# Kernel tuning notes

Hardware: AMD Instinct MI355X
Metric: run time of the kernel (lower is better)

Reference implementation:

```python
import jax, jax.numpy as jnp
import numpy as np


def setup_inputs() -> dict:
    key = jax.random.key(0)
    k1, k2 = jax.random.split(key)
    B, C, H, W = 8, 64, 128, 256
    left_feature = jax.random.normal(k1, (B, C, H, W), dtype=jnp.float32)
    right_feature = jax.random.normal(k2, (B, C, H, W), dtype=jnp.float32)
    return {
        "left_feature": left_feature,
        "right_feature": right_feature,
        "max_disp": 64,
    }


def reference(left_feature, right_feature, max_disp):
    # Stereo correlation cost volume (norm=False branch):
    #   volume[b, d, h, w] = mean_c( left[b,c,h,w] * right[b,c,h,w-d] )  for w >= d
    #   volume[b, d, h, w] = 0                                           for w <  d
    b, c, h, w = left_feature.shape

    def corr_at_disp(d):
        # left[:, :, :, d:] * right[:, :, :, :w-d], mean over channel dim
        prod = left_feature[:, :, :, d:] * right_feature[:, :, :, : w - d]
        cv = jnp.mean(prod, axis=1)  # (b, h, w-d)
        # left-pad along width with zeros for invalid disparities
        return jnp.pad(cv, ((0, 0), (0, 0), (d, 0)))

    # max_disp is a static Python int; loop over disparity hyperparameter is static.
    volume = jnp.stack([corr_at_disp(d) for d in range(max_disp)], axis=1)
    return volume  # (b, max_disp, h, w)
```

## Files before the change

kernel.cpp:

```cpp
#include <hip/hip_runtime.h>

typedef _Float16 half8 __attribute__((ext_vector_type(8)));
typedef float floatx4 __attribute__((ext_vector_type(4)));

#define BB 8
#define CC 64
#define HH 128
#define WW 256
#define DD 64
#define KCH 32
#define LROWS WW
#define RROWS (WW + 64)

__global__ __launch_bounds__(256, 3)
void corr_volume_mfma(const float* __restrict__ left,
                      const float* __restrict__ right,
                      float* __restrict__ out) {
    __shared__ _Float16 Lb[LROWS * KCH];
    __shared__ _Float16 Rb[RROWS * KCH];

    const int tid  = threadIdx.x;
    const int lane = tid & 63;
    const int wv   = tid >> 6;
    const int n    = lane & 15;
    const int q    = lane >> 4;
    const int bh   = blockIdx.x;
    const int b    = bh >> 7;
    const int h    = bh & 127;

    const size_t chanStride = (size_t)HH * WW;
    const size_t rowBase    = (size_t)b * CC * chanStride + (size_t)h * WW;

    {
        half8 z;
        #pragma unroll
        for (int t = 0; t < 8; ++t) z[t] = (_Float16)0.0f;
        *(half8*)&Rb[tid * 8] = z;
    }

    floatx4 acc[4][5];
    #pragma unroll
    for (int t = 0; t < 4; ++t)
        #pragma unroll
        for (int u = 0; u < 5; ++u)
            #pragma unroll
            for (int r = 0; r < 4; ++r)
                acc[t][u][r] = 0.0f;

    const int wbase = wv * 64;
    const float* lcol = left  + rowBase + tid;
    const float* rcol = right + rowBase + tid;

    for (int ck = 0; ck < 2; ++ck) {
        __syncthreads();
        const int cb = ck * KCH;
        _Float16* Lrow = &Lb[tid * KCH];
        _Float16* Rrow = &Rb[(tid + 64) * KCH];
        #pragma unroll
        for (int g = 0; g < 4; ++g) {
            float lv[8], rv[8];
            #pragma unroll
            for (int t = 0; t < 8; ++t) {
                lv[t] = lcol[(size_t)(cb + g * 8 + t) * chanStride];
                rv[t] = rcol[(size_t)(cb + g * 8 + t) * chanStride];
            }
            half8 lh, rh;
            #pragma unroll
            for (int t = 0; t < 8; ++t) {
                lh[t] = (_Float16)lv[t];
                rh[t] = (_Float16)rv[t];
            }
            *(half8*)&Lrow[g * 8] = lh;
            *(half8*)&Rrow[g * 8] = rh;
        }
        __syncthreads();

        half8 bfrag[4], afrag[8];
        #pragma unroll
        for (int t = 0; t < 4; ++t)
            bfrag[t] = *(const half8*)&Lb[(wbase + t * 16 + n) * KCH + q * 8];
        #pragma unroll
        for (int a = 0; a < 8; ++a)
            afrag[a] = *(const half8*)&Rb[(wbase + a * 16 + n) * KCH + q * 8];
        #pragma unroll
        for (int t = 0; t < 4; ++t)
            #pragma unroll
            for (int u = 0; u < 5; ++u)
                acc[t][u] = __builtin_amdgcn_mfma_f32_16x16x32_f16(
                    afrag[t + u], bfrag[t], acc[t][u], 0, 0, 0);
    }

    const float scale = 1.0f / 64.0f;
    #pragma unroll
    for (int t = 0; t < 4; ++t) {
        const int w = wbase + t * 16 + n;
        #pragma unroll
        for (int u = 0; u < 5; ++u) {
            #pragma unroll
            for (int r = 0; r < 4; ++r) {
                const int mo = q * 4 + r;
                const int d  = 64 - 16 * u + n - mo;
                if (d >= 0 && d <= 63) {
                    out[(((size_t)b * DD + d) * HH + h) * WW + w] =
                        acc[t][u][r] * scale;
                }
            }
        }
    }
}

extern "C" void kernel_launch(void* const* d_in, const int* in_sizes, int n_in,
                              void* d_out, int out_size, void* d_ws, size_t ws_size,
                              hipStream_t stream) {
    const float* left  = (const float*)d_in[0];
    const float* right = (const float*)d_in[1];
    float* out = (float*)d_out;

    dim3 grid(BB * HH);
    dim3 block(256);
    corr_volume_mfma<<<grid, block, 0, stream>>>(left, right, out);
}
```

Measured before the change: 191.9 us.

## Vectorize global loads, stage all channels with swizzled LDS, use 512-thread blocks

Each thread now issues float4 loads over 8 channels up front and converts them to fp16 in a single staging pass covering all 64 channels. The LDS layout uses an XOR swizzle to reduce bank conflicts on fragment reads. Blocks grow to 8 waves, each computing 32 output columns. This removes the two-chunk loop and scalar loads, at the cost of more registers and LDS per block, which may limit occupancy.

```diff
diff --git a/kernel.cpp b/kernel.cpp
--- a/kernel.cpp
+++ b/kernel.cpp
@@ -8,22 +8,17 @@
 #define HH 128
 #define WW 256
 #define DD 64
-#define KCH 32
-#define LROWS WW
-#define RROWS (WW + 64)
 
-__global__ __launch_bounds__(256, 3)
+__global__ __launch_bounds__(512, 4)
 void corr_volume_mfma(const float* __restrict__ left,
                       const float* __restrict__ right,
                       float* __restrict__ out) {
-    __shared__ _Float16 Lb[LROWS * KCH];
-    __shared__ _Float16 Rb[RROWS * KCH];
+    __shared__ _Float16 Lb[256 * 64];
+    __shared__ _Float16 Rb[320 * 64];
 
     const int tid  = threadIdx.x;
     const int lane = tid & 63;
     const int wv   = tid >> 6;
-    const int n    = lane & 15;
-    const int q    = lane >> 4;
     const int bh   = blockIdx.x;
     const int b    = bh >> 7;
     const int h    = bh & 127;
@@ -31,59 +26,66 @@
     const size_t chanStride = (size_t)HH * WW;
     const size_t rowBase    = (size_t)b * CC * chanStride + (size_t)h * WW;
 
+    const int sw = lane * 4;
+    const int cg = wv;
+
+    const float* lp = left  + rowBase + (size_t)(cg * 8) * chanStride + sw;
+    const float* rp = right + rowBase + (size_t)(cg * 8) * chanStride + sw;
+
+    float4 lv[8], rv[8];
+    #pragma unroll
+    for (int cc = 0; cc < 8; ++cc) {
+        lv[cc] = *(const float4*)(lp + (size_t)cc * chanStride);
+        rv[cc] = *(const float4*)(rp + (size_t)cc * chanStride);
+    }
+
     {
-        half8 z;
-        #pragma unroll
-        for (int t = 0; t < 8; ++t) z[t] = (_Float16)0.0f;
+        half8 z = {0, 0, 0, 0, 0, 0, 0, 0};
         *(half8*)&Rb[tid * 8] = z;
     }
 
-    floatx4 acc[4][5];
+    const float* lf = (const float*)lv;
+    const float* rf = (const float*)rv;
     #pragma unroll
-    for (int t = 0; t < 4; ++t)
+    for (int s = 0; s < 4; ++s) {
+        const int w   = sw + s;
+        const int col = (cg ^ (w & 7)) * 8;
+        half8 lh, rh;
+        #pragma unroll
+        for (int cc = 0; cc < 8; ++cc) {
+            lh[cc] = (_Float16)lf[cc * 4 + s];
+            rh[cc] = (_Float16)rf[cc * 4 + s];
+        }
+        *(half8*)&Lb[w * 64 + col]        = lh;
+        *(half8*)&Rb[(w + 64) * 64 + col] = rh;
+    }
+    __syncthreads();
+
+    const int n     = lane & 15;
+    const int q     = lane >> 4;
+    const int wbase = wv * 32;
+
+    floatx4 acc[2][5];
+    #pragma unroll
+    for (int t = 0; t < 2; ++t)
         #pragma unroll
         for (int u = 0; u < 5; ++u)
             #pragma unroll
             for (int r = 0; r < 4; ++r)
                 acc[t][u][r] = 0.0f;
 
-    const int wbase = wv * 64;
-    const float* lcol = left  + rowBase + tid;
-    const float* rcol = right + rowBase + tid;
-
-    for (int ck = 0; ck < 2; ++ck) {
-        __syncthreads();
-        const int cb = ck * KCH;
-        _Float16* Lrow = &Lb[tid * KCH];
-        _Float16* Rrow = &Rb[(tid + 64) * KCH];
+    #pragma unroll
+    for (int kk = 0; kk < 2; ++kk) {
+        const int col = ((kk * 4 + q) ^ (n & 7)) * 8;
+        half8 bfrag[2], afrag[6];
         #pragma unroll
-        for (int g = 0; g < 4; ++g) {
-            float lv[8], rv[8];
-            #pragma unroll
-            for (int t = 0; t < 8; ++t) {
-                lv[t] = lcol[(size_t)(cb + g * 8 + t) * chanStride];
-                rv[t] = rcol[(size_t)(cb + g * 8 + t) * chanStride];
-            }
-            half8 lh, rh;
-            #pragma unroll
-            for (int t = 0; t < 8; ++t) {
-                lh[t] = (_Float16)lv[t];
-                rh[t] = (_Float16)rv[t];
-            }
-            *(half8*)&Lrow[g * 8] = lh;
-            *(half8*)&Rrow[g * 8] = rh;
-        }
-        __syncthreads();
-
-        half8 bfrag[4], afrag[8];
+        for (int t = 0; t < 2; ++t)
+            bfrag[t] = *(const half8*)&Lb[(wbase + t * 16 + n) * 64 + col];
         #pragma unroll
-        for (int t = 0; t < 4; ++t)
-            bfrag[t] = *(const half8*)&Lb[(wbase + t * 16 + n) * KCH + q * 8];
+        for (int a = 0; a < 6; ++a)
+            afrag[a] = *(const half8*)&Rb[(wbase + a * 16 + n) * 64 + col];
         #pragma unroll
-        for (int a = 0; a < 8; ++a)
-            afrag[a] = *(const half8*)&Rb[(wbase + a * 16 + n) * KCH + q * 8];
-        #pragma unroll
-        for (int t = 0; t < 4; ++t)
+        for (int t = 0; t < 2; ++t)
             #pragma unroll
             for (int u = 0; u < 5; ++u)
                 acc[t][u] = __builtin_amdgcn_mfma_f32_16x16x32_f16(
@@ -92,15 +94,14 @@
 
     const float scale = 1.0f / 64.0f;
     #pragma unroll
-    for (int t = 0; t < 4; ++t) {
+    for (int t = 0; t < 2; ++t) {
         const int w = wbase + t * 16 + n;
         #pragma unroll
         for (int u = 0; u < 5; ++u) {
             #pragma unroll
             for (int r = 0; r < 4; ++r) {
-                const int mo = q * 4 + r;
-                const int d  = 64 - 16 * u + n - mo;
-                if (d >= 0 && d <= 63) {
+                const int d = 64 - 16 * u + n - (q * 4 + r);
+                if (d >= 0 && d < DD) {
                     out[(((size_t)b * DD + d) * HH + h) * WW + w] =
                         acc[t][u][r] * scale;
                 }
@@ -117,6 +118,6 @@
     float* out = (float*)d_out;
 
     dim3 grid(BB * HH);
-    dim3 block(256);
+    dim3 block(512);
     corr_volume_mfma<<<grid, block, 0, stream>>>(left, right, out);
 }
```

Measured after the change: 189.3 us. Within noise of the previous version (-1.4%).
